# Performance work log

Hardware: AMD Instinct MI355X
Metric: run time of the kernel (lower is better)

## Reference

```python
import jax, jax.numpy as jnp
import numpy as np

WIN = 8
SHIFT = 4
HEADS = 6

def _rel_pos_index(w):
    coords = np.stack(np.meshgrid(np.arange(w), np.arange(w), indexing='ij'))  # (2,w,w)
    cf = coords.reshape(2, -1)
    rel = (cf[:, :, None] - cf[:, None, :]).transpose(1, 2, 0)  # (N,N,2)
    rel[:, :, 0] += w - 1
    rel[:, :, 1] += w - 1
    rel[:, :, 0] *= 2 * w - 1
    return rel.sum(-1)  # (N,N) int

def _attn_mask(H, W, w, s):
    img = np.zeros((H, W))
    slices = (slice(0, -w), slice(-w, -s), slice(-s, None))
    cnt = 0
    for hs in slices:
        for ws in slices:
            img[hs, ws] = cnt
            cnt += 1
    mw = img.reshape(H // w, w, W // w, w).transpose(0, 2, 1, 3).reshape(-1, w * w)  # (nW,N)
    am = mw[:, None, :] - mw[:, :, None]
    return np.where(am != 0, -100.0, 0.0).astype(np.float32)  # (nW,N,N)

def _ln(z, g, b):
    mu = z.mean(-1, keepdims=True)
    var = z.var(-1, keepdims=True)
    return (z - mu) / jnp.sqrt(var + 1e-5) * g + b

def setup_inputs() -> dict:
    key = jax.random.key(0)
    ks = jax.random.split(key, 8)
    C, HID = 192, 768
    sc = lambda fan: 1.0 / np.sqrt(fan)
    return {
        'x': jax.random.normal(ks[0], (4, 256, 256, C), jnp.float32),
        'qkv_w': jax.random.normal(ks[1], (3 * C, C), jnp.float32) * sc(C),
        'qkv_b': jnp.zeros((3 * C,), jnp.float32),
        'proj_w': jax.random.normal(ks[2], (C, C), jnp.float32) * sc(C),
        'proj_b': jnp.zeros((C,), jnp.float32),
        'rpb': jax.random.normal(ks[3], (225, HEADS), jnp.float32) * 0.02,
        'n1_w': jnp.ones((C,), jnp.float32),
        'n1_b': jnp.zeros((C,), jnp.float32),
        'n2_w': jnp.ones((C,), jnp.float32),
        'n2_b': jnp.zeros((C,), jnp.float32),
        'fc1_w': jax.random.normal(ks[4], (HID, C), jnp.float32) * sc(C),
        'fc1_b': jnp.zeros((HID,), jnp.float32),
        'fc2_w': jax.random.normal(ks[5], (C, HID), jnp.float32) * sc(HID),
        'fc2_b': jnp.zeros((C,), jnp.float32),
    }

def reference(x, qkv_w, qkv_b, proj_w, proj_b, rpb, n1_w, n1_b, n2_w, n2_b, fc1_w, fc1_b, fc2_w, fc2_b):
    B, H, W, C = x.shape
    N = WIN * WIN
    hd = C // HEADS
    scale = hd ** -0.5

    shortcut = x.reshape(B, H * W, C)
    z = _ln(shortcut, n1_w, n1_b).reshape(B, H, W, C)
    z = jnp.roll(z, (-SHIFT, -SHIFT), axis=(1, 2))

    # window partition -> (B*nW, N, C)
    xw = z.reshape(B, H // WIN, WIN, W // WIN, WIN, C).transpose(0, 1, 3, 2, 4, 5).reshape(-1, N, C)
    B_ = xw.shape[0]

    qkv = (xw @ qkv_w.T + qkv_b).reshape(B_, N, 3, HEADS, hd).transpose(2, 0, 3, 1, 4)
    q, k, v = qkv[0] * scale, qkv[1], qkv[2]
    attn = jnp.einsum('bhnd,bhmd->bhnm', q, k)  # (B_,H,N,N)

    idx = _rel_pos_index(WIN)
    bias = rpb[idx.reshape(-1)].reshape(N, N, HEADS).transpose(2, 0, 1)  # (H,N,N)
    attn = attn + bias[None]

    mask = jnp.asarray(_attn_mask(H, W, WIN, SHIFT))  # (nW,N,N)
    nW = mask.shape[0]
    attn = attn.reshape(B_ // nW, nW, HEADS, N, N) + mask[None, :, None]
    attn = jax.nn.softmax(attn, axis=-1).reshape(B_, HEADS, N, N)

    out = jnp.einsum('bhnm,bhmd->bhnd', attn, v).transpose(0, 2, 1, 3).reshape(B_, N, C)
    out = out @ proj_w.T + proj_b

    # window reverse
    out = out.reshape(B, H // WIN, W // WIN, WIN, WIN, C).transpose(0, 1, 3, 2, 4, 5).reshape(B, H, W, C)
    out = jnp.roll(out, (SHIFT, SHIFT), axis=(1, 2)).reshape(B, H * W, C)

    h = shortcut + out
    m = _ln(h, n2_w, n2_b)
    m = jax.nn.gelu(m @ fc1_w.T + fc1_b, approximate=False)
    m = m @ fc2_w.T + fc2_b
    return (h + m).reshape(B, H, W, C)
```

## Files before the change

kernel.cpp:

```cpp
#include <hip/hip_runtime.h>
#include <hip/hip_bf16.h>

typedef __attribute__((ext_vector_type(8))) __bf16 bf16x8;
typedef __attribute__((ext_vector_type(4))) float f32x4;
typedef __hip_bfloat16 bf16;

#define SCALE_Q 0.17677669529663687f

#define LDSP(p) ((__attribute__((address_space(3))) unsigned int*)(unsigned long long)(p))
#define GPTR(p) ((const __attribute__((address_space(1))) unsigned int*)(unsigned long long)(p))
#define GLD16(gp, lp) __builtin_amdgcn_global_load_lds(GPTR(gp), LDSP(lp), 16, 0, 0)

__device__ inline float gelu_f(float x) {
  const float ax = fabsf(x) * 0.70710678118654752f;
  const float t = __builtin_amdgcn_rcpf(__builtin_fmaf(0.3275911f, ax, 1.0f));
  const float poly = t * __builtin_fmaf(t, __builtin_fmaf(t, __builtin_fmaf(t,
                     __builtin_fmaf(t, 1.061405429f, -1.453152027f),
                     1.421413741f), -0.284496736f), 0.254829592f);
  const float er = __builtin_fmaf(-poly, __expf(-ax * ax), 1.0f);
  return 0.5f * x * (1.0f + copysignf(er, x));
}

__global__ void cvt_kernel(const float* __restrict__ in, bf16* __restrict__ out, int n) {
  int i = blockIdx.x * 256 + threadIdx.x;
  if (i < n) out[i] = __float2bfloat16(in[i]);
}

template<int K, int KC>
__global__ void cvt_frag_kernel(const float* __restrict__ in, bf16* __restrict__ out, int total) {
  int i = blockIdx.x * 256 + threadIdx.x;
  if (i < total) {
    const int n = i / K, k = i - n * K;
    out[((n >> 4) * KC + (k >> 5)) * 512 + ((k >> 3) & 3) * 128 + (n & 15) * 8 + (k & 7)] =
        __float2bfloat16(in[i]);
  }
}

__global__ __launch_bounds__(512, 2) void qkv_ln1(const float* __restrict__ x,
                                                  const float* __restrict__ n1w,
                                                  const float* __restrict__ n1b,
                                                  const bf16* __restrict__ qwt,
                                                  const float* __restrict__ qb,
                                                  bf16* __restrict__ outp) {
  __shared__ __align__(16) char Ab[24576];
  const int tid = threadIdx.x;
  const long m0 = (long)blockIdx.x * 64;
  const int lane = tid & 63, wid = tid >> 6;
  const int lg = lane >> 4, lr = lane & 15;

  #pragma unroll
  for (int t8 = 0; t8 < 8; t8++) {
    const int row = wid * 8 + t8;
    const long t = m0 + row;
    const int b_ = (int)(t >> 6), n = (int)(t & 63);
    const int b = b_ >> 10, wk = b_ & 1023, wi = wk >> 5, wj = wk & 31;
    const int hf = (wi * 8 + (n >> 3) + 4) & 255, wf = (wj * 8 + (n & 7) + 4) & 255;
    const long g = (((long)b * 256 + hf) * 256 + wf) * 192;
    const float x0 = x[g + lane], x1 = x[g + 64 + lane], x2 = x[g + 128 + lane];
    float s = x0 + x1 + x2;
    float s2 = x0 * x0 + x1 * x1 + x2 * x2;
    #pragma unroll
    for (int msk = 1; msk < 64; msk <<= 1) { s += __shfl_xor(s, msk); s2 += __shfl_xor(s2, msk); }
    const float mu = s * (1.0f / 192.0f);
    const float rstd = rsqrtf(s2 * (1.0f / 192.0f) - mu * mu + 1e-5f);
    #pragma unroll
    for (int p = 0; p < 3; p++) {
      const int ch = p * 64 + lane;
      const float xv = (p == 0) ? x0 : (p == 1) ? x1 : x2;
      const float v = (xv - mu) * rstd * n1w[ch] + n1b[ch];
      const int c = (ch >> 3) & 7;
      const int slot = c ^ (row & 7);
      *(unsigned short*)(Ab + p * 8192 + row * 128 + slot * 16 + (ch & 7) * 2) =
          __builtin_bit_cast(unsigned short, __float2bfloat16(v));
    }
  }
  __syncthreads();

  const int wrr = (wid >> 2) * 32;
  const int wcg = wid & 3;
  f32x4 acc[2][9];
  #pragma unroll
  for (int i = 0; i < 2; i++)
    #pragma unroll
    for (int j = 0; j < 9; j++) acc[i][j] = (f32x4){0.f, 0.f, 0.f, 0.f};

  const int c16base = wcg * 9;
  #pragma unroll
  for (int kc = 0; kc < 6; kc++) {
    const int q = kc >> 1;
    const int kk = (kc & 1) * 4 + lg;
    bf16x8 af[2], bfr[9];
    #pragma unroll
    for (int i = 0; i < 2; i++) {
      const int row = wrr + i * 16 + lr;
      af[i] = *(const bf16x8*)(Ab + q * 8192 + row * 128 + ((kk ^ (row & 7)) * 16));
    }
    #pragma unroll
    for (int j = 0; j < 9; j++)
      bfr[j] = *(const bf16x8*)(qwt + ((c16base + j) * 6 + kc) * 512 + lane * 8);
    #pragma unroll
    for (int i = 0; i < 2; i++)
      #pragma unroll
      for (int j = 0; j < 9; j++)
        acc[i][j] = __builtin_amdgcn_mfma_f32_16x16x32_bf16(af[i], bfr[j], acc[i][j], 0, 0, 0);
  }

  #pragma unroll
  for (int i = 0; i < 2; i++) {
    #pragma unroll
    for (int j = 0; j < 9; j++) {
      #pragma unroll
      for (int r = 0; r < 4; r++) {
        const long m = m0 + wrr + i * 16 + lg * 4 + r;
        const int cn = wcg * 144 + j * 16 + lr;
        float v = acc[i][j][r] + qb[cn];
        const long b_ = m >> 6; const int n = (int)(m & 63);
        const int which = cn / 192, rem = cn - which * 192, head = rem >> 5, d = rem & 31;
        if (which == 0) v *= SCALE_Q;
        outp[((b_ * 6 + head) * 3 + which) * 2048 + n * 32 + d] = __float2bfloat16(v);
      }
    }
  }
}

template<int EPI>
__global__ __launch_bounds__(512, 4) void gemm_bt(const bf16* __restrict__ A,
                                                  const bf16* __restrict__ Bw,
                                                  const float* __restrict__ bias,
                                                  int K, void* __restrict__ outp,
                                                  const float* __restrict__ aux1,
                                                  const float* __restrict__ aux2) {
  __shared__ __align__(16) bf16 Ald[128 * 64];
  __shared__ __align__(16) bf16 Bld[192 * 64];
  const int tid = threadIdx.x;
  const int n0 = blockIdx.x * 192;
  const long m0 = (long)blockIdx.y * 128;
  const int lane = tid & 63, wid = tid >> 6;
  const int wr = (wid >> 1) * 32, wc = (wid & 1) * 96;
  const int lg = lane >> 4, lr = lane & 15;
  const int l3 = lane >> 3, l7 = lane & 7;
  const int chunk = l7 ^ l3;

  const bf16* aptr = A + (m0 + wid * 16 + l3) * (long)K + chunk * 8;
  const bf16* bptr = Bw + (n0 + wid * 24 + l3) * (long)K + chunk * 8;
  char* alds = (char*)Ald + wid * 16 * 128;
  char* blds = (char*)Bld + wid * 24 * 128;
  const long rk8 = 8 * (long)K;

  f32x4 acc[2][6];
  #pragma unroll
  for (int i = 0; i < 2; i++)
    #pragma unroll
    for (int j = 0; j < 6; j++) acc[i][j] = (f32x4){0.f, 0.f, 0.f, 0.f};

  for (int k0 = 0; k0 < K; k0 += 64) {
    GLD16(aptr + k0, alds);
    GLD16(aptr + rk8 + k0, alds + 1024);
    GLD16(bptr + k0, blds);
    GLD16(bptr + rk8 + k0, blds + 1024);
    GLD16(bptr + 2 * rk8 + k0, blds + 2048);
    __syncthreads();
    #pragma unroll
    for (int ks = 0; ks < 2; ks++) {
      bf16x8 af[2], bfr[6];
      #pragma unroll
      for (int i = 0; i < 2; i++) {
        const int row = wr + i * 16 + lr;
        af[i] = *(const bf16x8*)((const char*)Ald + row * 128 + (((ks * 4 + lg) ^ (row & 7)) * 16));
      }
      #pragma unroll
      for (int j = 0; j < 6; j++) {
        const int row = wc + j * 16 + lr;
        bfr[j] = *(const bf16x8*)((const char*)Bld + row * 128 + (((ks * 4 + lg) ^ (row & 7)) * 16));
      }
      #pragma unroll
      for (int i = 0; i < 2; i++)
        #pragma unroll
        for (int j = 0; j < 6; j++)
          acc[i][j] = __builtin_amdgcn_mfma_f32_16x16x32_bf16(af[i], bfr[j], acc[i][j], 0, 0, 0);
    }
    __syncthreads();
  }

  #pragma unroll
  for (int i = 0; i < 2; i++) {
    #pragma unroll
    for (int j = 0; j < 6; j++) {
      #pragma unroll
      for (int r = 0; r < 4; r++) {
        const long m = m0 + wr + i * 16 + lg * 4 + r;
        const int cn = n0 + wc + j * 16 + lr;
        float v = acc[i][j][r] + bias[cn];
        if (EPI == 0) {
          const long b_ = m >> 6; const int n = (int)(m & 63);
          const int which = cn / 192, rem = cn - which * 192, head = rem >> 5, d = rem & 31;
          if (which == 0) v *= SCALE_Q;
          ((bf16*)outp)[((b_ * 6 + head) * 3 + which) * 2048 + n * 32 + d] = __float2bfloat16(v);
        } else {
          const long b_ = m >> 6; const int n = (int)(m & 63);
          const int b = (int)(b_ >> 10), wk = (int)(b_ & 1023), wi = wk >> 5, wj = wk & 31;
          const int i_ = n >> 3, j_ = n & 7;
          const int hf = (wi * 8 + i_ + 4) & 255, wf = (wj * 8 + j_ + 4) & 255;
          const long g = (((long)b * 256 + hf) * 256 + wf) * 192 + cn;
          ((float*)outp)[g] = aux1[g] + v;
        }
      }
    }
  }
}

__global__ __launch_bounds__(512, 2) void mlp_fused(const float* __restrict__ hbuf,
                                                    const float* __restrict__ n2w,
                                                    const float* __restrict__ n2b,
                                                    const bf16* __restrict__ w1t,
                                                    const float* __restrict__ b1,
                                                    const bf16* __restrict__ w2t,
                                                    const float* __restrict__ b2,
                                                    float* __restrict__ outp) {
  __shared__ __align__(16) char smem[122880];
  char* Ab = smem;
  char* G  = smem + 24576;

  const int tid = threadIdx.x;
  const long m0 = (long)blockIdx.x * 64;
  const int lane = tid & 63, wid = tid >> 6;
  const int lg = lane >> 4, lr = lane & 15;

  #pragma unroll
  for (int t8 = 0; t8 < 8; t8++) {
    const int row = wid * 8 + t8;
    const long g = (m0 + row) * 192;
    const float x0 = hbuf[g + lane], x1 = hbuf[g + 64 + lane], x2 = hbuf[g + 128 + lane];
    float s = x0 + x1 + x2;
    float s2 = x0 * x0 + x1 * x1 + x2 * x2;
    #pragma unroll
    for (int msk = 1; msk < 64; msk <<= 1) { s += __shfl_xor(s, msk); s2 += __shfl_xor(s2, msk); }
    const float mu = s * (1.0f / 192.0f);
    const float rstd = rsqrtf(s2 * (1.0f / 192.0f) - mu * mu + 1e-5f);
    #pragma unroll
    for (int p = 0; p < 3; p++) {
      const int ch = p * 64 + lane;
      const float xv = (p == 0) ? x0 : (p == 1) ? x1 : x2;
      const float v = (xv - mu) * rstd * n2w[ch] + n2b[ch];
      const int c = (ch >> 3) & 7;
      const int slot = c ^ (row & 7);
      *(unsigned short*)(Ab + p * 8192 + row * 128 + slot * 16 + (ch & 7) * 2) =
          __builtin_bit_cast(unsigned short, __float2bfloat16(v));
    }
  }
  __syncthreads();

  f32x4 acc1[4][6];
  #pragma unroll
  for (int i = 0; i < 4; i++)
    #pragma unroll
    for (int j = 0; j < 6; j++) acc1[i][j] = (f32x4){0.f, 0.f, 0.f, 0.f};

  const int c16base = wid * 6;
  #pragma unroll
  for (int kc = 0; kc < 6; kc++) {
    const int q = kc >> 1;
    const int kk = (kc & 1) * 4 + lg;
    bf16x8 af[4], bfr[6];
    #pragma unroll
    for (int i = 0; i < 4; i++) {
      const int row = i * 16 + lr;
      af[i] = *(const bf16x8*)(Ab + q * 8192 + row * 128 + ((kk ^ (row & 7)) * 16));
    }
    #pragma unroll
    for (int j = 0; j < 6; j++)
      bfr[j] = *(const bf16x8*)(w1t + ((c16base + j) * 6 + kc) * 512 + lane * 8);
    #pragma unroll
    for (int i = 0; i < 4; i++)
      #pragma unroll
      for (int j = 0; j < 6; j++)
        acc1[i][j] = __builtin_amdgcn_mfma_f32_16x16x32_bf16(af[i], bfr[j], acc1[i][j], 0, 0, 0);
  }

  #pragma unroll
  for (int j = 0; j < 6; j++) {
    const int n = wid * 96 + j * 16 + lr;
    const float bj = b1[n];
    const int c = n >> 3;
    #pragma unroll
    for (int i = 0; i < 4; i++) {
      #pragma unroll
      for (int r = 0; r < 4; r++) {
        const int m = i * 16 + lg * 4 + r;
        const int slot = (c & ~7) | ((c & 7) ^ (m & 7));
        *(unsigned short*)(G + m * 1536 + slot * 16 + (n & 7) * 2) =
            __builtin_bit_cast(unsigned short, __float2bfloat16(gelu_f(acc1[i][j][r] + bj)));
      }
    }
  }
  __syncthreads();

  const int wt = wid >> 2, wn = wid & 3;
  f32x4 acc2[2][3];
  #pragma unroll
  for (int i = 0; i < 2; i++)
    #pragma unroll
    for (int j = 0; j < 3; j++) acc2[i][j] = (f32x4){0.f, 0.f, 0.f, 0.f};

  for (int kt = 0; kt < 24; kt++) {
    const int c2 = kt * 4 + lg;
    bf16x8 af2[2], bfr2[3];
    #pragma unroll
    for (int i = 0; i < 2; i++) {
      const int grow = wt * 32 + i * 16 + lr;
      const int slot2 = (c2 & ~7) | ((c2 & 7) ^ (grow & 7));
      af2[i] = *(const bf16x8*)(G + grow * 1536 + slot2 * 16);
    }
    #pragma unroll
    for (int j = 0; j < 3; j++)
      bfr2[j] = *(const bf16x8*)(w2t + ((wn * 3 + j) * 24 + kt) * 512 + lane * 8);
    #pragma unroll
    for (int i = 0; i < 2; i++)
      #pragma unroll
      for (int j = 0; j < 3; j++)
        acc2[i][j] = __builtin_amdgcn_mfma_f32_16x16x32_bf16(af2[i], bfr2[j], acc2[i][j], 0, 0, 0);
  }

  #pragma unroll
  for (int j = 0; j < 3; j++) {
    const int cn = wn * 48 + j * 16 + lr;
    const float bj = b2[cn];
    #pragma unroll
    for (int i = 0; i < 2; i++) {
      #pragma unroll
      for (int r = 0; r < 4; r++) {
        const long m = m0 + wt * 32 + i * 16 + lg * 4 + r;
        outp[m * 192 + cn] = acc2[i][j][r] + bj + hbuf[m * 192 + cn];
      }
    }
  }
}

__global__ __launch_bounds__(64) void attn_kernel(const bf16* __restrict__ qkv,
                                                  const float* __restrict__ rpb,
                                                  bf16* __restrict__ outp) {
  __shared__ __align__(16) char smem[14848];
  __shared__ float rps[225];
  const int bid = blockIdx.x;
  const int b_ = bid / 6, head = bid - b_ * 6;
  const int lane = threadIdx.x;
  const long base = ((long)b_ * 6 + head) * 3 * 2048;

  for (int t = lane; t < 225; t += 64) rps[t] = rpb[t * 6 + head];

  #pragma unroll
  for (int q = 0; q < 4; q++) {
    const int f = q * 64 + lane, row = f >> 2, c = f & 3;
    *(uint4*)(smem + row * 80 + c * 16) = *(const uint4*)(qkv + base + row * 32 + c * 8);
    *(uint4*)(smem + 5120 + row * 80 + c * 16) = *(const uint4*)(qkv + base + 2048 + row * 32 + c * 8);
  }
  {
    const bf16* vsrc = qkv + base + 4096 + lane * 32;
    bf16 vv[32];
    #pragma unroll
    for (int q = 0; q < 4; q++) *(uint4*)&vv[q * 8] = *(const uint4*)(vsrc + q * 8);
    bf16* vt = (bf16*)(smem + 10240);
    #pragma unroll
    for (int d = 0; d < 32; d++) vt[d * 72 + lane] = vv[d];
  }
  __syncthreads();

  const int lg = lane >> 4, lr = lane & 15;
  const f32x4 z4 = {0.f, 0.f, 0.f, 0.f};
  f32x4 s[4][4];
  {
    bf16x8 a[4], b[4];
    #pragma unroll
    for (int fi = 0; fi < 4; fi++)
      a[fi] = *(const bf16x8*)(smem + (fi * 16 + lr) * 80 + lg * 16);
    #pragma unroll
    for (int fj = 0; fj < 4; fj++)
      b[fj] = *(const bf16x8*)(smem + 5120 + (fj * 16 + lr) * 80 + lg * 16);
    #pragma unroll
    for (int fi = 0; fi < 4; fi++)
      #pragma unroll
      for (int fj = 0; fj < 4; fj++)
        s[fi][fj] = __builtin_amdgcn_mfma_f32_16x16x32_bf16(a[fi], b[fj], z4, 0, 0, 0);
  }

  const int wk = b_ & 1023; const int wi = wk >> 5, wj = wk & 31;
  const bool eh = (wi == 31), ew = (wj == 31);
  bf16* P = (bf16*)smem;
  #pragma unroll
  for (int fi = 0; fi < 4; fi++) {
    #pragma unroll
    for (int r = 0; r < 4; r++) {
      const int n = fi * 16 + lg * 4 + r;
      const int i1 = n >> 3, j1 = n & 7;
      const int labn = (eh ? (i1 < 4 ? 3 : 6) : 0) + (ew ? (j1 < 4 ? 1 : 2) : 0);
      float vals[4];
      #pragma unroll
      for (int fj = 0; fj < 4; fj++) {
        const int m = fj * 16 + lr;
        const int i2 = m >> 3, j2 = m & 7;
        const int labm = (eh ? (i2 < 4 ? 3 : 6) : 0) + (ew ? (j2 < 4 ? 1 : 2) : 0);
        vals[fj] = s[fi][fj][r] + rps[(i1 - i2 + 7) * 15 + (j1 - j2 + 7)]
                 + (labn != labm ? -100.0f : 0.0f);
      }
      float mx = fmaxf(fmaxf(vals[0], vals[1]), fmaxf(vals[2], vals[3]));
      #pragma unroll
      for (int msk = 1; msk < 16; msk <<= 1) mx = fmaxf(mx, __shfl_xor(mx, msk));
      float pe[4]; float sum = 0.f;
      #pragma unroll
      for (int fj = 0; fj < 4; fj++) { pe[fj] = __expf(vals[fj] - mx); sum += pe[fj]; }
      #pragma unroll
      for (int msk = 1; msk < 16; msk <<= 1) sum += __shfl_xor(sum, msk);
      const float rinv = 1.0f / sum;
      #pragma unroll
      for (int fj = 0; fj < 4; fj++)
        P[n * 72 + fj * 16 + lr] = __float2bfloat16(pe[fj] * rinv);
    }
  }
  __syncthreads();

  f32x4 o[4][2];
  #pragma unroll
  for (int fi = 0; fi < 4; fi++)
    #pragma unroll
    for (int fd = 0; fd < 2; fd++) o[fi][fd] = z4;
  const bf16* vt = (const bf16*)(smem + 10240);
  #pragma unroll
  for (int ks = 0; ks < 2; ks++) {
    bf16x8 pa[4], vb[2];
    #pragma unroll
    for (int fi = 0; fi < 4; fi++)
      pa[fi] = *(const bf16x8*)(P + (fi * 16 + lr) * 72 + ks * 32 + lg * 8);
    #pragma unroll
    for (int fd = 0; fd < 2; fd++)
      vb[fd] = *(const bf16x8*)(vt + (fd * 16 + lr) * 72 + ks * 32 + lg * 8);
    #pragma unroll
    for (int fi = 0; fi < 4; fi++)
      #pragma unroll
      for (int fd = 0; fd < 2; fd++)
        o[fi][fd] = __builtin_amdgcn_mfma_f32_16x16x32_bf16(pa[fi], vb[fd], o[fi][fd], 0, 0, 0);
  }
  #pragma unroll
  for (int fi = 0; fi < 4; fi++)
    #pragma unroll
    for (int fd = 0; fd < 2; fd++)
      #pragma unroll
      for (int r = 0; r < 4; r++) {
        const int n = fi * 16 + lg * 4 + r;
        outp[((long)b_ * 64 + n) * 192 + head * 32 + fd * 16 + lr] = __float2bfloat16(o[fi][fd][r]);
      }
}

extern "C" void kernel_launch(void* const* d_in, const int* in_sizes, int n_in,
                              void* d_out, int out_size, void* d_ws, size_t ws_size,
                              hipStream_t stream) {
  const float* x      = (const float*)d_in[0];
  const float* qkv_w  = (const float*)d_in[1];
  const float* qkv_b  = (const float*)d_in[2];
  const float* proj_w = (const float*)d_in[3];
  const float* proj_b = (const float*)d_in[4];
  const float* rpb    = (const float*)d_in[5];
  const float* n1_w   = (const float*)d_in[6];
  const float* n1_b   = (const float*)d_in[7];
  const float* n2_w   = (const float*)d_in[8];
  const float* n2_b   = (const float*)d_in[9];
  const float* fc1_w  = (const float*)d_in[10];
  const float* fc1_b  = (const float*)d_in[11];
  const float* fc2_w  = (const float*)d_in[12];
  const float* fc2_b  = (const float*)d_in[13];

  char* ws = (char*)d_ws;
  bf16* qkvw_t  = (bf16*)(ws);
  bf16* projw_h = (bf16*)(ws + 221184);
  bf16* fc1w_t  = (bf16*)(ws + 294912);
  bf16* fc2w_t  = (bf16*)(ws + 589824);
  bf16* r1      = (bf16*)(ws + (1L << 20));
  bf16* r2      = (bf16*)(ws + 101711872L);
  float* hbuf   = (float*)(ws + 504365056L);

  cvt_frag_kernel<192, 6><<<432, 256, 0, stream>>>(qkv_w, qkvw_t, 110592);
  cvt_kernel<<<144, 256, 0, stream>>>(proj_w, projw_h, 36864);
  cvt_frag_kernel<192, 6><<<576, 256, 0, stream>>>(fc1_w, fc1w_t, 147456);
  cvt_frag_kernel<768, 24><<<576, 256, 0, stream>>>(fc2_w, fc2w_t, 147456);

  qkv_ln1<<<4096, 512, 0, stream>>>(x, n1_w, n1_b, qkvw_t, qkv_b, r2);
  attn_kernel<<<24576, 64, 0, stream>>>(r2, rpb, r1);
  gemm_bt<1><<<dim3(1, 2048), 512, 0, stream>>>(r1, projw_h, proj_b, 192, hbuf, x, nullptr);
  mlp_fused<<<4096, 512, 0, stream>>>(hbuf, n2_w, n2_b, fc1w_t, fc1_b, fc2w_t, fc2_b,
                                      (float*)d_out);
}
```

Before: 803.8 us.

## Fuse LN1, QKV projection, window attention and output projection into one kernel

Replaces the separate qkv_ln1, attn_kernel and gemm_bt launches with a single per-window kernel. Q, K and V stay in LDS, attention runs one head per wave, and the attention output is written back into the swizzled A tile. The proj GEMM then uses pre-fragmented weights and adds the residual directly into hbuf. This removes the global round trips of the large bf16 qkv and attention-output intermediates. In exchange, the roughly 119KB LDS footprint limits occupancy to about one block per CU, and two of the eight waves sit idle during the attention stage.

After: 802.1 us. No clear change (-0.2%).

```diff
diff --git a/kernel.cpp b/kernel.cpp
--- a/kernel.cpp
+++ b/kernel.cpp
@@ -6,10 +6,6 @@
 typedef __hip_bfloat16 bf16;
 
 #define SCALE_Q 0.17677669529663687f
-
-#define LDSP(p) ((__attribute__((address_space(3))) unsigned int*)(unsigned long long)(p))
-#define GPTR(p) ((const __attribute__((address_space(1))) unsigned int*)(unsigned long long)(p))
-#define GLD16(gp, lp) __builtin_amdgcn_global_load_lds(GPTR(gp), LDSP(lp), 16, 0, 0)
 
 __device__ inline float gelu_f(float x) {
   const float ax = fabsf(x) * 0.70710678118654752f;
@@ -21,11 +17,6 @@
   return 0.5f * x * (1.0f + copysignf(er, x));
 }
 
-__global__ void cvt_kernel(const float* __restrict__ in, bf16* __restrict__ out, int n) {
-  int i = blockIdx.x * 256 + threadIdx.x;
-  if (i < n) out[i] = __float2bfloat16(in[i]);
-}
-
 template<int K, int KC>
 __global__ void cvt_frag_kernel(const float* __restrict__ in, bf16* __restrict__ out, int total) {
   int i = blockIdx.x * 256 + threadIdx.x;
@@ -36,17 +27,32 @@
   }
 }
 
-__global__ __launch_bounds__(512, 2) void qkv_ln1(const float* __restrict__ x,
-                                                  const float* __restrict__ n1w,
-                                                  const float* __restrict__ n1b,
-                                                  const bf16* __restrict__ qwt,
-                                                  const float* __restrict__ qb,
-                                                  bf16* __restrict__ outp) {
-  __shared__ __align__(16) char Ab[24576];
+__global__ __launch_bounds__(512, 2) void win_attn(const float* __restrict__ x,
+                                                   const float* __restrict__ n1w,
+                                                   const float* __restrict__ n1b,
+                                                   const bf16* __restrict__ qwt,
+                                                   const float* __restrict__ qb,
+                                                   const float* __restrict__ rpb,
+                                                   const bf16* __restrict__ pwt,
+                                                   const float* __restrict__ pb,
+                                                   float* __restrict__ hbuf) {
+  __shared__ __align__(16) char smem[119072];
+  char* Qt = smem;
+  char* Kt = smem + 30720;
+  char* Vtb = smem + 61440;
+  char* Ab = smem + 89088;
+  float* rpl = (float*)(smem + 113664);
+
   const int tid = threadIdx.x;
-  const long m0 = (long)blockIdx.x * 64;
+  const int blk = blockIdx.x;
+  const long m0 = (long)blk * 64;
   const int lane = tid & 63, wid = tid >> 6;
   const int lg = lane >> 4, lr = lane & 15;
+
+  for (int t = tid; t < 1350; t += 512) {
+    const int hh = t / 225, tt = t - hh * 225;
+    rpl[hh * 225 + tt] = rpb[tt * 6 + hh];
+  }
 
   #pragma unroll
   for (int t8 = 0; t8 < 8; t8++) {
@@ -76,133 +82,194 @@
   }
   __syncthreads();
 
-  const int wrr = (wid >> 2) * 32;
-  const int wcg = wid & 3;
-  f32x4 acc[2][9];
-  #pragma unroll
-  for (int i = 0; i < 2; i++)
-    #pragma unroll
-    for (int j = 0; j < 9; j++) acc[i][j] = (f32x4){0.f, 0.f, 0.f, 0.f};
-
-  const int c16base = wcg * 9;
-  #pragma unroll
-  for (int kc = 0; kc < 6; kc++) {
-    const int q = kc >> 1;
-    const int kk = (kc & 1) * 4 + lg;
-    bf16x8 af[2], bfr[9];
+  {
+    const int wrr = (wid >> 2) * 32;
+    const int wcg = wid & 3;
+    f32x4 acc[2][9];
+    #pragma unroll
+    for (int i = 0; i < 2; i++)
+      #pragma unroll
+      for (int j = 0; j < 9; j++) acc[i][j] = (f32x4){0.f, 0.f, 0.f, 0.f};
+    const int c16base = wcg * 9;
+    #pragma unroll
+    for (int kc = 0; kc < 6; kc++) {
+      const int q = kc >> 1;
+      const int kk = (kc & 1) * 4 + lg;
+      bf16x8 af[2], bfr[9];
+      #pragma unroll
+      for (int i = 0; i < 2; i++) {
+        const int row = wrr + i * 16 + lr;
+        af[i] = *(const bf16x8*)(Ab + q * 8192 + row * 128 + ((kk ^ (row & 7)) * 16));
+      }
+      #pragma unroll
+      for (int j = 0; j < 9; j++)
+        bfr[j] = *(const bf16x8*)(qwt + ((c16base + j) * 6 + kc) * 512 + lane * 8);
+      #pragma unroll
+      for (int i = 0; i < 2; i++)
+        #pragma unroll
+        for (int j = 0; j < 9; j++)
+          acc[i][j] = __builtin_amdgcn_mfma_f32_16x16x32_bf16(af[i], bfr[j], acc[i][j], 0, 0, 0);
+    }
+    __syncthreads();
     #pragma unroll
     for (int i = 0; i < 2; i++) {
-      const int row = wrr + i * 16 + lr;
-      af[i] = *(const bf16x8*)(Ab + q * 8192 + row * 128 + ((kk ^ (row & 7)) * 16));
-    }
-    #pragma unroll
-    for (int j = 0; j < 9; j++)
-      bfr[j] = *(const bf16x8*)(qwt + ((c16base + j) * 6 + kc) * 512 + lane * 8);
+      #pragma unroll
+      for (int j = 0; j < 9; j++) {
+        #pragma unroll
+        for (int r = 0; r < 4; r++) {
+          const int n = wrr + i * 16 + lg * 4 + r;
+          const int cn = wcg * 144 + j * 16 + lr;
+          float v = acc[i][j][r] + qb[cn];
+          const int which = cn / 192, rem = cn - which * 192, head = rem >> 5, d = rem & 31;
+          unsigned short us;
+          if (which == 0) { v *= SCALE_Q; us = __builtin_bit_cast(unsigned short, __float2bfloat16(v));
+            *(unsigned short*)(Qt + head * 5120 + n * 80 + d * 2) = us; }
+          else if (which == 1) { us = __builtin_bit_cast(unsigned short, __float2bfloat16(v));
+            *(unsigned short*)(Kt + head * 5120 + n * 80 + d * 2) = us; }
+          else { us = __builtin_bit_cast(unsigned short, __float2bfloat16(v));
+            *(unsigned short*)(Vtb + head * 4608 + (d * 72 + n) * 2) = us; }
+        }
+      }
+    }
+  }
+  __syncthreads();
+
+  const f32x4 z4 = {0.f, 0.f, 0.f, 0.f};
+  f32x4 s[4][4];
+  const int head = wid;
+  if (wid < 6) {
+    bf16x8 a[4], b[4];
+    #pragma unroll
+    for (int fi = 0; fi < 4; fi++)
+      a[fi] = *(const bf16x8*)(Qt + head * 5120 + (fi * 16 + lr) * 80 + lg * 16);
+    #pragma unroll
+    for (int fj = 0; fj < 4; fj++)
+      b[fj] = *(const bf16x8*)(Kt + head * 5120 + (fj * 16 + lr) * 80 + lg * 16);
+    #pragma unroll
+    for (int fi = 0; fi < 4; fi++)
+      #pragma unroll
+      for (int fj = 0; fj < 4; fj++)
+        s[fi][fj] = __builtin_amdgcn_mfma_f32_16x16x32_bf16(a[fi], b[fj], z4, 0, 0, 0);
+  }
+  __syncthreads();
+
+  bf16* P = (bf16*)(smem + head * 9216);
+  if (wid < 6) {
+    const int wk = blk & 1023; const int wi = wk >> 5, wj = wk & 31;
+    const bool eh = (wi == 31), ew = (wj == 31);
+    const float* rps = rpl + head * 225;
+    #pragma unroll
+    for (int fi = 0; fi < 4; fi++) {
+      #pragma unroll
+      for (int r = 0; r < 4; r++) {
+        const int n = fi * 16 + lg * 4 + r;
+        const int i1 = n >> 3, j1 = n & 7;
+        const int labn = (eh ? (i1 < 4 ? 3 : 6) : 0) + (ew ? (j1 < 4 ? 1 : 2) : 0);
+        float vals[4];
+        #pragma unroll
+        for (int fj = 0; fj < 4; fj++) {
+          const int m = fj * 16 + lr;
+          const int i2 = m >> 3, j2 = m & 7;
+          const int labm = (eh ? (i2 < 4 ? 3 : 6) : 0) + (ew ? (j2 < 4 ? 1 : 2) : 0);
+          vals[fj] = s[fi][fj][r] + rps[(i1 - i2 + 7) * 15 + (j1 - j2 + 7)]
+                   + (labn != labm ? -100.0f : 0.0f);
+        }
+        float mx = fmaxf(fmaxf(vals[0], vals[1]), fmaxf(vals[2], vals[3]));
+        #pragma unroll
+        for (int msk = 1; msk < 16; msk <<= 1) mx = fmaxf(mx, __shfl_xor(mx, msk));
+        float pe[4]; float sum = 0.f;
+        #pragma unroll
+        for (int fj = 0; fj < 4; fj++) { pe[fj] = __expf(vals[fj] - mx); sum += pe[fj]; }
+        #pragma unroll
+        for (int msk = 1; msk < 16; msk <<= 1) sum += __shfl_xor(sum, msk);
+        const float rinv = 1.0f / sum;
+        #pragma unroll
+        for (int fj = 0; fj < 4; fj++)
+          P[n * 72 + fj * 16 + lr] = __float2bfloat16(pe[fj] * rinv);
+      }
+    }
+  }
+  __syncthreads();
+
+  if (wid < 6) {
+    f32x4 o[4][2];
+    #pragma unroll
+    for (int fi = 0; fi < 4; fi++)
+      #pragma unroll
+      for (int fd = 0; fd < 2; fd++) o[fi][fd] = z4;
+    const bf16* vt = (const bf16*)(Vtb + head * 4608);
+    #pragma unroll
+    for (int ks = 0; ks < 2; ks++) {
+      bf16x8 pa[4], vb[2];
+      #pragma unroll
+      for (int fi = 0; fi < 4; fi++)
+        pa[fi] = *(const bf16x8*)(P + (fi * 16 + lr) * 72 + ks * 32 + lg * 8);
+      #pragma unroll
+      for (int fd = 0; fd < 2; fd++)
+        vb[fd] = *(const bf16x8*)(vt + (fd * 16 + lr) * 72 + ks * 32 + lg * 8);
+      #pragma unroll
+      for (int fi = 0; fi < 4; fi++)
+        #pragma unroll
+        for (int fd = 0; fd < 2; fd++)
+          o[fi][fd] = __builtin_amdgcn_mfma_f32_16x16x32_bf16(pa[fi], vb[fd], o[fi][fd], 0, 0, 0);
+    }
+    #pragma unroll
+    for (int fi = 0; fi < 4; fi++)
+      #pragma unroll
+      for (int fd = 0; fd < 2; fd++)
+        #pragma unroll
+        for (int r = 0; r < 4; r++) {
+          const int n = fi * 16 + lg * 4 + r;
+          const int ch = head * 32 + fd * 16 + lr;
+          const int p = ch >> 6, c = (ch >> 3) & 7;
+          const int slot = c ^ (n & 7);
+          *(unsigned short*)(Ab + p * 8192 + n * 128 + slot * 16 + (ch & 7) * 2) =
+              __builtin_bit_cast(unsigned short, __float2bfloat16(o[fi][fd][r]));
+        }
+  }
+  __syncthreads();
+
+  {
+    const int wrr2 = (wid >> 2) * 32, wcg2 = wid & 3;
+    f32x4 accp[2][3];
     #pragma unroll
     for (int i = 0; i < 2; i++)
       #pragma unroll
-      for (int j = 0; j < 9; j++)
-        acc[i][j] = __builtin_amdgcn_mfma_f32_16x16x32_bf16(af[i], bfr[j], acc[i][j], 0, 0, 0);
-  }
-
-  #pragma unroll
-  for (int i = 0; i < 2; i++) {
-    #pragma unroll
-    for (int j = 0; j < 9; j++) {
-      #pragma unroll
-      for (int r = 0; r < 4; r++) {
-        const long m = m0 + wrr + i * 16 + lg * 4 + r;
-        const int cn = wcg * 144 + j * 16 + lr;
-        float v = acc[i][j][r] + qb[cn];
-        const long b_ = m >> 6; const int n = (int)(m & 63);
-        const int which = cn / 192, rem = cn - which * 192, head = rem >> 5, d = rem & 31;
-        if (which == 0) v *= SCALE_Q;
-        outp[((b_ * 6 + head) * 3 + which) * 2048 + n * 32 + d] = __float2bfloat16(v);
-      }
-    }
-  }
-}
-
-template<int EPI>
-__global__ __launch_bounds__(512, 4) void gemm_bt(const bf16* __restrict__ A,
-                                                  const bf16* __restrict__ Bw,
-                                                  const float* __restrict__ bias,
-                                                  int K, void* __restrict__ outp,
-                                                  const float* __restrict__ aux1,
-                                                  const float* __restrict__ aux2) {
-  __shared__ __align__(16) bf16 Ald[128 * 64];
-  __shared__ __align__(16) bf16 Bld[192 * 64];
-  const int tid = threadIdx.x;
-  const int n0 = blockIdx.x * 192;
-  const long m0 = (long)blockIdx.y * 128;
-  const int lane = tid & 63, wid = tid >> 6;
-  const int wr = (wid >> 1) * 32, wc = (wid & 1) * 96;
-  const int lg = lane >> 4, lr = lane & 15;
-  const int l3 = lane >> 3, l7 = lane & 7;
-  const int chunk = l7 ^ l3;
-
-  const bf16* aptr = A + (m0 + wid * 16 + l3) * (long)K + chunk * 8;
-  const bf16* bptr = Bw + (n0 + wid * 24 + l3) * (long)K + chunk * 8;
-  char* alds = (char*)Ald + wid * 16 * 128;
-  char* blds = (char*)Bld + wid * 24 * 128;
-  const long rk8 = 8 * (long)K;
-
-  f32x4 acc[2][6];
-  #pragma unroll
-  for (int i = 0; i < 2; i++)
-    #pragma unroll
-    for (int j = 0; j < 6; j++) acc[i][j] = (f32x4){0.f, 0.f, 0.f, 0.f};
-
-  for (int k0 = 0; k0 < K; k0 += 64) {
-    GLD16(aptr + k0, alds);
-    GLD16(aptr + rk8 + k0, alds + 1024);
-    GLD16(bptr + k0, blds);
-    GLD16(bptr + rk8 + k0, blds + 1024);
-    GLD16(bptr + 2 * rk8 + k0, blds + 2048);
-    __syncthreads();
-    #pragma unroll
-    for (int ks = 0; ks < 2; ks++) {
-      bf16x8 af[2], bfr[6];
+      for (int j = 0; j < 3; j++) accp[i][j] = (f32x4){0.f, 0.f, 0.f, 0.f};
+    #pragma unroll
+    for (int kc = 0; kc < 6; kc++) {
+      const int q = kc >> 1;
+      const int kk = (kc & 1) * 4 + lg;
+      bf16x8 af[2], bfr[3];
       #pragma unroll
       for (int i = 0; i < 2; i++) {
-        const int row = wr + i * 16 + lr;
-        af[i] = *(const bf16x8*)((const char*)Ald + row * 128 + (((ks * 4 + lg) ^ (row & 7)) * 16));
-      }
-      #pragma unroll
-      for (int j = 0; j < 6; j++) {
-        const int row = wc + j * 16 + lr;
-        bfr[j] = *(const bf16x8*)((const char*)Bld + row * 128 + (((ks * 4 + lg) ^ (row & 7)) * 16));
-      }
+        const int row = wrr2 + i * 16 + lr;
+        af[i] = *(const bf16x8*)(Ab + q * 8192 + row * 128 + ((kk ^ (row & 7)) * 16));
+      }
+      #pragma unroll
+      for (int j = 0; j < 3; j++)
+        bfr[j] = *(const bf16x8*)(pwt + ((wcg2 * 3 + j) * 6 + kc) * 512 + lane * 8);
       #pragma unroll
       for (int i = 0; i < 2; i++)
         #pragma unroll
-        for (int j = 0; j < 6; j++)
-          acc[i][j] = __builtin_amdgcn_mfma_f32_16x16x32_bf16(af[i], bfr[j], acc[i][j], 0, 0, 0);
-    }
-    __syncthreads();
-  }
-
-  #pragma unroll
-  for (int i = 0; i < 2; i++) {
-    #pragma unroll
-    for (int j = 0; j < 6; j++) {
-      #pragma unroll
-      for (int r = 0; r < 4; r++) {
-        const long m = m0 + wr + i * 16 + lg * 4 + r;
-        const int cn = n0 + wc + j * 16 + lr;
-        float v = acc[i][j][r] + bias[cn];
-        if (EPI == 0) {
-          const long b_ = m >> 6; const int n = (int)(m & 63);
-          const int which = cn / 192, rem = cn - which * 192, head = rem >> 5, d = rem & 31;
-          if (which == 0) v *= SCALE_Q;
-          ((bf16*)outp)[((b_ * 6 + head) * 3 + which) * 2048 + n * 32 + d] = __float2bfloat16(v);
-        } else {
+        for (int j = 0; j < 3; j++)
+          accp[i][j] = __builtin_amdgcn_mfma_f32_16x16x32_bf16(af[i], bfr[j], accp[i][j], 0, 0, 0);
+    }
+    #pragma unroll
+    for (int i = 0; i < 2; i++) {
+      #pragma unroll
+      for (int j = 0; j < 3; j++) {
+        #pragma unroll
+        for (int r = 0; r < 4; r++) {
+          const long m = m0 + wrr2 + i * 16 + lg * 4 + r;
+          const int cn = wcg2 * 48 + j * 16 + lr;
+          const float v = accp[i][j][r] + pb[cn];
           const long b_ = m >> 6; const int n = (int)(m & 63);
           const int b = (int)(b_ >> 10), wk = (int)(b_ & 1023), wi = wk >> 5, wj = wk & 31;
           const int i_ = n >> 3, j_ = n & 7;
           const int hf = (wi * 8 + i_ + 4) & 255, wf = (wj * 8 + j_ + 4) & 255;
           const long g = (((long)b * 256 + hf) * 256 + wf) * 192 + cn;
-          ((float*)outp)[g] = aux1[g] + v;
+          hbuf[g] = x[g] + v;
         }
       }
     }
@@ -334,120 +401,6 @@
       }
     }
   }
-}
-
-__global__ __launch_bounds__(64) void attn_kernel(const bf16* __restrict__ qkv,
-                                                  const float* __restrict__ rpb,
-                                                  bf16* __restrict__ outp) {
-  __shared__ __align__(16) char smem[14848];
-  __shared__ float rps[225];
-  const int bid = blockIdx.x;
-  const int b_ = bid / 6, head = bid - b_ * 6;
-  const int lane = threadIdx.x;
-  const long base = ((long)b_ * 6 + head) * 3 * 2048;
-
-  for (int t = lane; t < 225; t += 64) rps[t] = rpb[t * 6 + head];
-
-  #pragma unroll
-  for (int q = 0; q < 4; q++) {
-    const int f = q * 64 + lane, row = f >> 2, c = f & 3;
-    *(uint4*)(smem + row * 80 + c * 16) = *(const uint4*)(qkv + base + row * 32 + c * 8);
-    *(uint4*)(smem + 5120 + row * 80 + c * 16) = *(const uint4*)(qkv + base + 2048 + row * 32 + c * 8);
-  }
-  {
-    const bf16* vsrc = qkv + base + 4096 + lane * 32;
-    bf16 vv[32];
-    #pragma unroll
-    for (int q = 0; q < 4; q++) *(uint4*)&vv[q * 8] = *(const uint4*)(vsrc + q * 8);
-    bf16* vt = (bf16*)(smem + 10240);
-    #pragma unroll
-    for (int d = 0; d < 32; d++) vt[d * 72 + lane] = vv[d];
-  }
-  __syncthreads();
-
-  const int lg = lane >> 4, lr = lane & 15;
-  const f32x4 z4 = {0.f, 0.f, 0.f, 0.f};
-  f32x4 s[4][4];
-  {
-    bf16x8 a[4], b[4];
-    #pragma unroll
-    for (int fi = 0; fi < 4; fi++)
-      a[fi] = *(const bf16x8*)(smem + (fi * 16 + lr) * 80 + lg * 16);
-    #pragma unroll
-    for (int fj = 0; fj < 4; fj++)
-      b[fj] = *(const bf16x8*)(smem + 5120 + (fj * 16 + lr) * 80 + lg * 16);
-    #pragma unroll
-    for (int fi = 0; fi < 4; fi++)
-      #pragma unroll
-      for (int fj = 0; fj < 4; fj++)
-        s[fi][fj] = __builtin_amdgcn_mfma_f32_16x16x32_bf16(a[fi], b[fj], z4, 0, 0, 0);
-  }
-
-  const int wk = b_ & 1023; const int wi = wk >> 5, wj = wk & 31;
-  const bool eh = (wi == 31), ew = (wj == 31);
-  bf16* P = (bf16*)smem;
-  #pragma unroll
-  for (int fi = 0; fi < 4; fi++) {
-    #pragma unroll
-    for (int r = 0; r < 4; r++) {
-      const int n = fi * 16 + lg * 4 + r;
-      const int i1 = n >> 3, j1 = n & 7;
-      const int labn = (eh ? (i1 < 4 ? 3 : 6) : 0) + (ew ? (j1 < 4 ? 1 : 2) : 0);
-      float vals[4];
-      #pragma unroll
-      for (int fj = 0; fj < 4; fj++) {
-        const int m = fj * 16 + lr;
-        const int i2 = m >> 3, j2 = m & 7;
-        const int labm = (eh ? (i2 < 4 ? 3 : 6) : 0) + (ew ? (j2 < 4 ? 1 : 2) : 0);
-        vals[fj] = s[fi][fj][r] + rps[(i1 - i2 + 7) * 15 + (j1 - j2 + 7)]
-                 + (labn != labm ? -100.0f : 0.0f);
-      }
-      float mx = fmaxf(fmaxf(vals[0], vals[1]), fmaxf(vals[2], vals[3]));
-      #pragma unroll
-      for (int msk = 1; msk < 16; msk <<= 1) mx = fmaxf(mx, __shfl_xor(mx, msk));
-      float pe[4]; float sum = 0.f;
-      #pragma unroll
-      for (int fj = 0; fj < 4; fj++) { pe[fj] = __expf(vals[fj] - mx); sum += pe[fj]; }
-      #pragma unroll
-      for (int msk = 1; msk < 16; msk <<= 1) sum += __shfl_xor(sum, msk);
-      const float rinv = 1.0f / sum;
-      #pragma unroll
-      for (int fj = 0; fj < 4; fj++)
-        P[n * 72 + fj * 16 + lr] = __float2bfloat16(pe[fj] * rinv);
-    }
-  }
-  __syncthreads();
-
-  f32x4 o[4][2];
-  #pragma unroll
-  for (int fi = 0; fi < 4; fi++)
-    #pragma unroll
-    for (int fd = 0; fd < 2; fd++) o[fi][fd] = z4;
-  const bf16* vt = (const bf16*)(smem + 10240);
-  #pragma unroll
-  for (int ks = 0; ks < 2; ks++) {
-    bf16x8 pa[4], vb[2];
-    #pragma unroll
-    for (int fi = 0; fi < 4; fi++)
-      pa[fi] = *(const bf16x8*)(P + (fi * 16 + lr) * 72 + ks * 32 + lg * 8);
-    #pragma unroll
-    for (int fd = 0; fd < 2; fd++)
-      vb[fd] = *(const bf16x8*)(vt + (fd * 16 + lr) * 72 + ks * 32 + lg * 8);
-    #pragma unroll
-    for (int fi = 0; fi < 4; fi++)
-      #pragma unroll
-      for (int fd = 0; fd < 2; fd++)
-        o[fi][fd] = __builtin_amdgcn_mfma_f32_16x16x32_bf16(pa[fi], vb[fd], o[fi][fd], 0, 0, 0);
-  }
-  #pragma unroll
-  for (int fi = 0; fi < 4; fi++)
-    #pragma unroll
-    for (int fd = 0; fd < 2; fd++)
-      #pragma unroll
-      for (int r = 0; r < 4; r++) {
-        const int n = fi * 16 + lg * 4 + r;
-        outp[((long)b_ * 64 + n) * 192 + head * 32 + fd * 16 + lr] = __float2bfloat16(o[fi][fd][r]);
-      }
 }
 
 extern "C" void kernel_launch(void* const* d_in, const int* in_sizes, int n_in,
@@ -470,21 +423,17 @@
 
   char* ws = (char*)d_ws;
   bf16* qkvw_t  = (bf16*)(ws);
-  bf16* projw_h = (bf16*)(ws + 221184);
+  bf16* projw_t = (bf16*)(ws + 221184);
   bf16* fc1w_t  = (bf16*)(ws + 294912);
   bf16* fc2w_t  = (bf16*)(ws + 589824);
-  bf16* r1      = (bf16*)(ws + (1L << 20));
-  bf16* r2      = (bf16*)(ws + 101711872L);
-  float* hbuf   = (float*)(ws + 504365056L);
+  float* hbuf   = (float*)(ws + (1L << 20));
 
   cvt_frag_kernel<192, 6><<<432, 256, 0, stream>>>(qkv_w, qkvw_t, 110592);
-  cvt_kernel<<<144, 256, 0, stream>>>(proj_w, projw_h, 36864);
+  cvt_frag_kernel<192, 6><<<144, 256, 0, stream>>>(proj_w, projw_t, 36864);
   cvt_frag_kernel<192, 6><<<576, 256, 0, stream>>>(fc1_w, fc1w_t, 147456);
   cvt_frag_kernel<768, 24><<<576, 256, 0, stream>>>(fc2_w, fc2w_t, 147456);
 
-  qkv_ln1<<<4096, 512, 0, stream>>>(x, n1_w, n1_b, qkvw_t, qkv_b, r2);
-  attn_kernel<<<24576, 64, 0, stream>>>(r2, rpb, r1);
-  gemm_bt<1><<<dim3(1, 2048), 512, 0, stream>>>(r1, projw_h, proj_b, 192, hbuf, x, nullptr);
+  win_attn<<<4096, 512, 0, stream>>>(x, n1_w, n1_b, qkvw_t, qkv_b, rpb, projw_t, proj_b, hbuf);
   mlp_fused<<<4096, 512, 0, stream>>>(hbuf, n2_w, n2_b, fc1w_t, fc1_b, fc2w_t, fc2_b,
                                       (float*)d_out);
 }
```
